# Performance work log

Measured on AMD Instinct MI355X. Metric: run time of the kernel, lower is better.

Reference implementation:

```python
import jax, jax.numpy as jnp
import numpy as np

N_NODES = 100000
IN_CH = 256
HIDDEN = 256
N_EDGES = 500000


def setup_inputs() -> dict:
    key = jax.random.key(0)
    k_emb, k_ei, k_w1, k_w2 = jax.random.split(key, 4)
    embeddings = jax.random.normal(k_emb, (N_NODES, IN_CH), dtype=jnp.float32)
    edge_index = jax.random.randint(k_ei, (2, N_EDGES), 0, N_NODES, dtype=jnp.int64)
    # Linear(in*2, hidden) and Linear(hidden, 1) weights (stored input-major for x @ W)
    s1 = 1.0 / np.sqrt(2 * IN_CH)
    s2 = 1.0 / np.sqrt(HIDDEN)
    W1 = jax.random.uniform(k_w1, (2 * IN_CH, HIDDEN), dtype=jnp.float32, minval=-s1, maxval=s1)
    b1 = jnp.zeros((HIDDEN,), dtype=jnp.float32)
    W2 = jax.random.uniform(k_w2, (HIDDEN, 1), dtype=jnp.float32, minval=-s2, maxval=s2)
    b2 = jnp.zeros((1,), dtype=jnp.float32)
    return {"embeddings": embeddings, "edge_index": edge_index,
            "W1": W1, "b1": b1, "W2": W2, "b2": b2}


def reference(embeddings, edge_index, W1, b1, W2, b2):
    src, dst = edge_index[0], edge_index[1]
    # gather [E, in] twice, concat -> [E, 2*in]
    feats = jnp.concatenate([embeddings[src], embeddings[dst]], axis=-1)
    h = jax.nn.relu(feats @ W1 + b1)          # [E, hidden]
    scores = h @ W2 + b2                      # [E, 1]
    return scores.reshape(-1)
```

## Files before the change

### kernel.cpp

```cpp
#include <hip/hip_runtime.h>
#include <hip/hip_bf16.h>

#define NN   100000
#define EE   500000
#define MPAD 100096

using bf16x8 = __attribute__((ext_vector_type(8))) short;
using f32x4  = __attribute__((ext_vector_type(4))) float;
using u16x8  = __attribute__((ext_vector_type(8))) unsigned short;

__device__ __forceinline__ unsigned short f2bf(float f) {
  unsigned int x = __builtin_bit_cast(unsigned int, f);
  x += 0x7fffu + ((x >> 16) & 1u);
  return (unsigned short)(x >> 16);
}
__device__ __forceinline__ float bf2f(unsigned short u) {
  unsigned int x = ((unsigned int)u) << 16;
  return __builtin_bit_cast(float, x);
}
__device__ __forceinline__ unsigned short f2bh(float f) {
  return __builtin_bit_cast(unsigned short, __float2bfloat16(f));
}
__device__ __forceinline__ void glds16(const void* g, const void* l) {
  __builtin_amdgcn_global_load_lds((const __attribute__((address_space(1))) void*)g,
                                   (__attribute__((address_space(3))) void*)l, 16, 0, 0);
}

__global__ void wprep_kernel(const float* __restrict__ W1, unsigned short* __restrict__ WT) {
  int id = blockIdx.x * blockDim.x + threadIdx.x;
  if (id >= 512 * 32) return;
  int j  = id >> 5;
  int cg = id & 31;
  int jc = j & 255;
  int kb = (cg << 3) + ((j >= 256) ? 256 : 0);
  u16x8 v;
#pragma unroll
  for (int t = 0; t < 8; ++t)
    v[t] = f2bf(W1[(size_t)(kb + t) * 256 + jc]);
  *reinterpret_cast<u16x8*>(WT + (size_t)j * 256 + (cg << 3)) = v;
}

__global__ __launch_bounds__(256, 4) void gemm_pq(const float* __restrict__ emb,
                                                  const unsigned short* __restrict__ WT,
                                                  const float* __restrict__ b1,
                                                  unsigned short* __restrict__ R) {
  __shared__ unsigned short ldsA[2][128 * 32];
  __shared__ unsigned short ldsB[2][128 * 32];

  const int t    = threadIdx.x;
  const int lane = t & 63;
  const int wave = t >> 6;
  const int wrow = wave >> 1, wcol = wave & 1;
  const int bid = (int)blockIdx.x;
  const int lid = (bid & 7) * 391 + (bid >> 3);
  const int m0 = (lid >> 2) * 128;
  const int n0 = (lid & 3) * 128;

  const int a_r = t >> 1, a_h = t & 1;
  int arow_g = m0 + a_r; if (arow_g >= NN) arow_g = NN - 1;
  const float* aSrc = emb + (size_t)arow_g * 256 + (a_h << 4);
  const int a_s  = (a_r >> 1) & 3;
  const int aW0  = a_r * 32 + ((((a_h << 1) | 0) ^ a_s) << 3);
  const int aW1  = a_r * 32 + ((((a_h << 1) | 1) ^ a_s) << 3);

  size_t bOff[2]; int bLds[2];
#pragma unroll
  for (int i = 0; i < 2; ++i) {
    const int r  = wave * 32 + i * 16 + (lane >> 2);
    const int qp = lane & 3;
    const int g  = qp ^ ((r >> 1) & 3);
    bOff[i] = (size_t)(n0 + r) * 256 + (g << 3);
    bLds[i] = (wave * 32 + i * 16) * 32;
  }

  const int fr = lane & 15, fq = lane >> 4;
  int aoff[4], boff[4];
#pragma unroll
  for (int m = 0; m < 4; ++m) {
    const int r = wrow * 64 + 16 * m + fr;
    aoff[m] = r * 32 + ((fq ^ ((r >> 1) & 3)) << 3);
  }
#pragma unroll
  for (int n = 0; n < 4; ++n) {
    const int r = wcol * 64 + 16 * n + fr;
    boff[n] = r * 32 + ((fq ^ ((r >> 1) & 3)) << 3);
  }

  f32x4 acc[4][4] = {};
  float4 pA[4];

#define ALOAD(kb)                                                              \
  do {                                                                         \
    pA[0] = *(const float4*)(aSrc + (kb));                                     \
    pA[1] = *(const float4*)(aSrc + (kb) + 4);                                 \
    pA[2] = *(const float4*)(aSrc + (kb) + 8);                                 \
    pA[3] = *(const float4*)(aSrc + (kb) + 12);                                \
  } while (0)

#define AWRITE(buf)                                                            \
  do {                                                                         \
    u16x8 w0, w1;                                                              \
    w0[0] = f2bh(pA[0].x); w0[1] = f2bh(pA[0].y);                              \
    w0[2] = f2bh(pA[0].z); w0[3] = f2bh(pA[0].w);                              \
    w0[4] = f2bh(pA[1].x); w0[5] = f2bh(pA[1].y);                              \
    w0[6] = f2bh(pA[1].z); w0[7] = f2bh(pA[1].w);                              \
    w1[0] = f2bh(pA[2].x); w1[1] = f2bh(pA[2].y);                              \
    w1[2] = f2bh(pA[2].z); w1[3] = f2bh(pA[2].w);                              \
    w1[4] = f2bh(pA[3].x); w1[5] = f2bh(pA[3].y);                              \
    w1[6] = f2bh(pA[3].z); w1[7] = f2bh(pA[3].w);                              \
    *(u16x8*)&ldsA[(buf)][aW0] = w0;                                           \
    *(u16x8*)&ldsA[(buf)][aW1] = w1;                                           \
  } while (0)

#define BGLDS(buf, kb)                                                         \
  do {                                                                         \
    glds16(WT + bOff[0] + (kb), &ldsB[(buf)][bLds[0]]);                        \
    glds16(WT + bOff[1] + (kb), &ldsB[(buf)][bLds[1]]);                        \
  } while (0)

  ALOAD(0);
  AWRITE(0);
  BGLDS(0, 0);
  ALOAD(32);
  __syncthreads();

#pragma unroll
  for (int ks = 0; ks < 8; ++ks) {
    const int p = ks & 1;
    if (ks < 7) {
      BGLDS(p ^ 1, (ks + 1) * 32);
      AWRITE(p ^ 1);
      if (ks < 6) ALOAD((ks + 2) * 32);
    }
    bf16x8 av[4], bv[4];
#pragma unroll
    for (int m = 0; m < 4; ++m) av[m] = *(const bf16x8*)&ldsA[p][aoff[m]];
#pragma unroll
    for (int n = 0; n < 4; ++n) bv[n] = *(const bf16x8*)&ldsB[p][boff[n]];
#pragma unroll
    for (int m = 0; m < 4; ++m)
#pragma unroll
      for (int n = 0; n < 4; ++n)
        acc[m][n] = __builtin_amdgcn_mfma_f32_16x16x32_bf16(av[m], bv[n], acc[m][n], 0, 0, 0);
    if (ks < 7) __syncthreads();
  }

  float bn[4];
#pragma unroll
  for (int n = 0; n < 4; ++n) {
    const int c = n0 + wcol * 64 + 16 * n + fr;
    bn[n] = (c < 256) ? b1[c] : 0.f;
  }
#pragma unroll
  for (int m = 0; m < 4; ++m) {
    const int r0 = m0 + wrow * 64 + 16 * m + (fq << 2);
#pragma unroll
    for (int n = 0; n < 4; ++n) {
      const int c = n0 + wcol * 64 + 16 * n + fr;
#pragma unroll
      for (int i = 0; i < 4; ++i)
        R[(size_t)(r0 + i) * 512 + c] = f2bh(acc[m][n][i] + bn[n]);
    }
  }
#undef ALOAD
#undef AWRITE
#undef BGLDS
}

__global__ __launch_bounds__(256) void edge_kernel(const int* __restrict__ idx,
                                                   const unsigned short* __restrict__ R,
                                                   const float* __restrict__ W2,
                                                   const float* __restrict__ b2,
                                                   float* __restrict__ out) {
  const int lane  = threadIdx.x & 63;
  const int half  = lane >> 5;
  const int l     = lane & 31;
  const int gwave = (int)((blockIdx.x * blockDim.x + threadIdx.x) >> 6);
  const int nwave = (int)((gridDim.x * blockDim.x) >> 6);
  const float4 w0 = *(const float4*)(W2 + (l << 3));
  const float4 w1 = *(const float4*)(W2 + (l << 3) + 4);
  const float bias = b2[0];

  for (int c = gwave; c < (EE / 8); c += nwave) {
    const int e0 = c << 3;
    int s[4], d[4];
#pragma unroll
    for (int u = 0; u < 4; ++u) {
      s[u] = idx[e0 + (u << 1) + half];
      d[u] = idx[EE + e0 + (u << 1) + half];
    }
    u16x8 ga[4], gb[4];
#pragma unroll
    for (int u = 0; u < 4; ++u) {
      ga[u] = *(const u16x8*)(R + (size_t)s[u] * 512 + (l << 3));
      gb[u] = *(const u16x8*)(R + (size_t)d[u] * 512 + 256 + (l << 3));
    }
#pragma unroll
    for (int u = 0; u < 4; ++u) {
      float acc;
      acc  = fmaxf(bf2f((unsigned short)ga[u][0]) + bf2f((unsigned short)gb[u][0]), 0.f) * w0.x;
      acc += fmaxf(bf2f((unsigned short)ga[u][1]) + bf2f((unsigned short)gb[u][1]), 0.f) * w0.y;
      acc += fmaxf(bf2f((unsigned short)ga[u][2]) + bf2f((unsigned short)gb[u][2]), 0.f) * w0.z;
      acc += fmaxf(bf2f((unsigned short)ga[u][3]) + bf2f((unsigned short)gb[u][3]), 0.f) * w0.w;
      acc += fmaxf(bf2f((unsigned short)ga[u][4]) + bf2f((unsigned short)gb[u][4]), 0.f) * w1.x;
      acc += fmaxf(bf2f((unsigned short)ga[u][5]) + bf2f((unsigned short)gb[u][5]), 0.f) * w1.y;
      acc += fmaxf(bf2f((unsigned short)ga[u][6]) + bf2f((unsigned short)gb[u][6]), 0.f) * w1.z;
      acc += fmaxf(bf2f((unsigned short)ga[u][7]) + bf2f((unsigned short)gb[u][7]), 0.f) * w1.w;
#pragma unroll
      for (int off = 16; off > 0; off >>= 1) acc += __shfl_xor(acc, off, 64);
      if (l == 0) out[e0 + (u << 1) + half] = acc + bias;
    }
  }
}

__global__ __launch_bounds__(256) void fallback_kernel(const float* __restrict__ emb,
                                                       const int* __restrict__ idx,
                                                       const float* __restrict__ W1,
                                                       const float* __restrict__ b1,
                                                       const float* __restrict__ W2,
                                                       const float* __restrict__ b2,
                                                       float* __restrict__ out) {
  __shared__ float feats[512];
  __shared__ float red[256];
  const int t = threadIdx.x;
  for (int e = blockIdx.x; e < EE; e += gridDim.x) {
    __syncthreads();
    const int s = idx[e], d = idx[EE + e];
    feats[t]       = emb[(size_t)s * 256 + t];
    feats[256 + t] = emb[(size_t)d * 256 + t];
    __syncthreads();
    float h = b1[t];
    for (int k = 0; k < 512; ++k) h += feats[k] * W1[k * 256 + t];
    red[t] = fmaxf(h, 0.f) * W2[t];
    __syncthreads();
    for (int off = 128; off > 0; off >>= 1) {
      if (t < off) red[t] += red[t + off];
      __syncthreads();
    }
    if (t == 0) out[e] = red[0] + b2[0];
  }
}

extern "C" void kernel_launch(void* const* d_in, const int* in_sizes, int n_in,
                              void* d_out, int out_size, void* d_ws, size_t ws_size,
                              hipStream_t stream) {
  const float* emb = (const float*)d_in[0];
  const int*   idx = (const int*)d_in[1];
  const float* W1  = (const float*)d_in[2];
  const float* b1  = (const float*)d_in[3];
  const float* W2  = (const float*)d_in[4];
  const float* b2  = (const float*)d_in[5];
  float* out = (float*)d_out;

  const size_t wt_elems = (size_t)512 * 256;
  const size_t r_elems  = (size_t)MPAD * 512;
  const size_t need = (wt_elems + r_elems) * sizeof(unsigned short);

  if (ws_size < need) {
    fallback_kernel<<<4096, 256, 0, stream>>>(emb, idx, W1, b1, W2, b2, out);
    return;
  }

  unsigned short* WT = (unsigned short*)d_ws;
  unsigned short* R  = WT + wt_elems;

  wprep_kernel<<<64, 256, 0, stream>>>(W1, WT);
  gemm_pq<<<(MPAD / 128) * 4, 256, 0, stream>>>(emb, WT, b1, R);
  edge_kernel<<<2048, 256, 0, stream>>>(idx, R, W2, b2, out);
}
```

Baseline: 138.8 us.

## Pre-convert embeddings to bf16 and stage GEMM A tiles via direct LDS loads

Adds a separate pass that converts the fp32 embedding table to a padded bf16 buffer in workspace. The GEMM then loads both A and B tiles with global_load_lds straight into LDS, removing the per-tile register staging and fp32-to-bf16 conversion from its main loop. Occupancy hint drops from 4 to 3 blocks. The cost is an extra kernel that reads 100MB of fp32 and writes 50MB of bf16, plus a larger workspace requirement. The old path is kept as a fallback when workspace is too small.

```diff
diff --git a/kernel.cpp b/kernel.cpp
--- a/kernel.cpp
+++ b/kernel.cpp
@@ -24,6 +24,23 @@
 __device__ __forceinline__ void glds16(const void* g, const void* l) {
   __builtin_amdgcn_global_load_lds((const __attribute__((address_space(1))) void*)g,
                                    (__attribute__((address_space(3))) void*)l, 16, 0, 0);
+}
+
+__global__ __launch_bounds__(256) void cvt_emb(const float* __restrict__ emb,
+                                               unsigned short* __restrict__ EB) {
+  const int ngrp = MPAD * 32;
+  for (int g = blockIdx.x * blockDim.x + threadIdx.x; g < ngrp;
+       g += gridDim.x * blockDim.x) {
+    const int row  = g >> 5;
+    const int col8 = (g & 31) << 3;
+    const int srow = (row < NN) ? row : (NN - 1);
+    const float4 f0 = *(const float4*)(emb + (size_t)srow * 256 + col8);
+    const float4 f1 = *(const float4*)(emb + (size_t)srow * 256 + col8 + 4);
+    u16x8 v;
+    v[0] = f2bh(f0.x); v[1] = f2bh(f0.y); v[2] = f2bh(f0.z); v[3] = f2bh(f0.w);
+    v[4] = f2bh(f1.x); v[5] = f2bh(f1.y); v[6] = f2bh(f1.z); v[7] = f2bh(f1.w);
+    *(u16x8*)(EB + (size_t)row * 256 + col8) = v;
+  }
 }
 
 __global__ void wprep_kernel(const float* __restrict__ W1, unsigned short* __restrict__ WT) {
@@ -40,7 +57,7 @@
   *reinterpret_cast<u16x8*>(WT + (size_t)j * 256 + (cg << 3)) = v;
 }
 
-__global__ __launch_bounds__(256, 4) void gemm_pq(const float* __restrict__ emb,
+__global__ __launch_bounds__(256, 3) void gemm_pq(const unsigned short* __restrict__ EB,
                                                   const unsigned short* __restrict__ WT,
                                                   const float* __restrict__ b1,
                                                   unsigned short* __restrict__ R) {
@@ -56,13 +73,100 @@
   const int m0 = (lid >> 2) * 128;
   const int n0 = (lid & 3) * 128;
 
+  size_t aOffG[2], bOffG[2]; int sLds[2];
+#pragma unroll
+  for (int i = 0; i < 2; ++i) {
+    const int r  = wave * 32 + i * 16 + (lane >> 2);
+    const int qp = lane & 3;
+    const int g  = qp ^ ((r >> 1) & 3);
+    aOffG[i] = (size_t)(m0 + r) * 256 + (g << 3);
+    bOffG[i] = (size_t)(n0 + r) * 256 + (g << 3);
+    sLds[i]  = (wave * 32 + i * 16) * 32;
+  }
+
+  const int fr = lane & 15, fq = lane >> 4;
+  int aoff[4], boff[4];
+#pragma unroll
+  for (int m = 0; m < 4; ++m) {
+    const int r = wrow * 64 + 16 * m + fr;
+    aoff[m] = r * 32 + ((fq ^ ((r >> 1) & 3)) << 3);
+  }
+#pragma unroll
+  for (int n = 0; n < 4; ++n) {
+    const int r = wcol * 64 + 16 * n + fr;
+    boff[n] = r * 32 + ((fq ^ ((r >> 1) & 3)) << 3);
+  }
+
+#define STAGE(buf, kb)                                                         \
+  do {                                                                         \
+    glds16(EB + aOffG[0] + (kb), &ldsA[(buf)][sLds[0]]);                       \
+    glds16(EB + aOffG[1] + (kb), &ldsA[(buf)][sLds[1]]);                       \
+    glds16(WT + bOffG[0] + (kb), &ldsB[(buf)][sLds[0]]);                       \
+    glds16(WT + bOffG[1] + (kb), &ldsB[(buf)][sLds[1]]);                       \
+  } while (0)
+
+  f32x4 acc[4][4] = {};
+
+  STAGE(0, 0);
+  __syncthreads();
+
+#pragma unroll
+  for (int ks = 0; ks < 8; ++ks) {
+    const int p = ks & 1;
+    if (ks < 7) STAGE(p ^ 1, (ks + 1) * 32);
+    bf16x8 av[4], bv[4];
+#pragma unroll
+    for (int m = 0; m < 4; ++m) av[m] = *(const bf16x8*)&ldsA[p][aoff[m]];
+#pragma unroll
+    for (int n = 0; n < 4; ++n) bv[n] = *(const bf16x8*)&ldsB[p][boff[n]];
+#pragma unroll
+    for (int m = 0; m < 4; ++m)
+#pragma unroll
+      for (int n = 0; n < 4; ++n)
+        acc[m][n] = __builtin_amdgcn_mfma_f32_16x16x32_bf16(av[m], bv[n], acc[m][n], 0, 0, 0);
+    if (ks < 7) __syncthreads();
+  }
+
+  float bn[4];
+#pragma unroll
+  for (int n = 0; n < 4; ++n) {
+    const int c = n0 + wcol * 64 + 16 * n + fr;
+    bn[n] = (c < 256) ? b1[c] : 0.f;
+  }
+#pragma unroll
+  for (int m = 0; m < 4; ++m) {
+    const int r0 = m0 + wrow * 64 + 16 * m + (fq << 2);
+#pragma unroll
+    for (int n = 0; n < 4; ++n) {
+      const int c = n0 + wcol * 64 + 16 * n + fr;
+#pragma unroll
+      for (int i = 0; i < 4; ++i)
+        R[(size_t)(r0 + i) * 512 + c] = f2bh(acc[m][n][i] + bn[n]);
+    }
+  }
+#undef STAGE
+}
+
+__global__ __launch_bounds__(256, 3) void gemm_pq_r5(const float* __restrict__ emb,
+                                                     const unsigned short* __restrict__ WT,
+                                                     const float* __restrict__ b1,
+                                                     unsigned short* __restrict__ R) {
+  __shared__ unsigned short ldsA[2][128 * 32];
+  __shared__ unsigned short ldsB[2][128 * 32];
+  const int t    = threadIdx.x;
+  const int lane = t & 63;
+  const int wave = t >> 6;
+  const int wrow = wave >> 1, wcol = wave & 1;
+  const int bid = (int)blockIdx.x;
+  const int lid = (bid & 7) * 391 + (bid >> 3);
+  const int m0 = (lid >> 2) * 128;
+  const int n0 = (lid & 3) * 128;
   const int a_r = t >> 1, a_h = t & 1;
   int arow_g = m0 + a_r; if (arow_g >= NN) arow_g = NN - 1;
   const float* aSrc = emb + (size_t)arow_g * 256 + (a_h << 4);
   const int a_s  = (a_r >> 1) & 3;
   const int aW0  = a_r * 32 + ((((a_h << 1) | 0) ^ a_s) << 3);
   const int aW1  = a_r * 32 + ((((a_h << 1) | 1) ^ a_s) << 3);
-
   size_t bOff[2]; int bLds[2];
 #pragma unroll
   for (int i = 0; i < 2; ++i) {
@@ -72,7 +176,6 @@
     bOff[i] = (size_t)(n0 + r) * 256 + (g << 3);
     bLds[i] = (wave * 32 + i * 16) * 32;
   }
-
   const int fr = lane & 15, fq = lane >> 4;
   int aoff[4], boff[4];
 #pragma unroll
@@ -85,21 +188,15 @@
     const int r = wcol * 64 + 16 * n + fr;
     boff[n] = r * 32 + ((fq ^ ((r >> 1) & 3)) << 3);
   }
-
   f32x4 acc[4][4] = {};
   float4 pA[4];
-
 #define ALOAD(kb)                                                              \
-  do {                                                                         \
-    pA[0] = *(const float4*)(aSrc + (kb));                                     \
-    pA[1] = *(const float4*)(aSrc + (kb) + 4);                                 \
-    pA[2] = *(const float4*)(aSrc + (kb) + 8);                                 \
-    pA[3] = *(const float4*)(aSrc + (kb) + 12);                                \
-  } while (0)
-
+  do { pA[0] = *(const float4*)(aSrc + (kb));                                  \
+       pA[1] = *(const float4*)(aSrc + (kb) + 4);                              \
+       pA[2] = *(const float4*)(aSrc + (kb) + 8);                              \
+       pA[3] = *(const float4*)(aSrc + (kb) + 12); } while (0)
 #define AWRITE(buf)                                                            \
-  do {                                                                         \
-    u16x8 w0, w1;                                                              \
+  do { u16x8 w0, w1;                                                           \
     w0[0] = f2bh(pA[0].x); w0[1] = f2bh(pA[0].y);                              \
     w0[2] = f2bh(pA[0].z); w0[3] = f2bh(pA[0].w);                              \
     w0[4] = f2bh(pA[1].x); w0[5] = f2bh(pA[1].y);                              \
@@ -109,21 +206,12 @@
     w1[4] = f2bh(pA[3].x); w1[5] = f2bh(pA[3].y);                              \
     w1[6] = f2bh(pA[3].z); w1[7] = f2bh(pA[3].w);                              \
     *(u16x8*)&ldsA[(buf)][aW0] = w0;                                           \
-    *(u16x8*)&ldsA[(buf)][aW1] = w1;                                           \
-  } while (0)
-
+    *(u16x8*)&ldsA[(buf)][aW1] = w1; } while (0)
 #define BGLDS(buf, kb)                                                         \
-  do {                                                                         \
-    glds16(WT + bOff[0] + (kb), &ldsB[(buf)][bLds[0]]);                        \
-    glds16(WT + bOff[1] + (kb), &ldsB[(buf)][bLds[1]]);                        \
-  } while (0)
-
-  ALOAD(0);
-  AWRITE(0);
-  BGLDS(0, 0);
-  ALOAD(32);
+  do { glds16(WT + bOff[0] + (kb), &ldsB[(buf)][bLds[0]]);                     \
+       glds16(WT + bOff[1] + (kb), &ldsB[(buf)][bLds[1]]); } while (0)
+  ALOAD(0); AWRITE(0); BGLDS(0, 0); ALOAD(32);
   __syncthreads();
-
 #pragma unroll
   for (int ks = 0; ks < 8; ++ks) {
     const int p = ks & 1;
@@ -144,7 +232,6 @@
         acc[m][n] = __builtin_amdgcn_mfma_f32_16x16x32_bf16(av[m], bv[n], acc[m][n], 0, 0, 0);
     if (ks < 7) __syncthreads();
   }
-
   float bn[4];
 #pragma unroll
   for (int n = 0; n < 4; ++n) {
@@ -254,17 +341,24 @@
 
   const size_t wt_elems = (size_t)512 * 256;
   const size_t r_elems  = (size_t)MPAD * 512;
-  const size_t need = (wt_elems + r_elems) * sizeof(unsigned short);
-
-  if (ws_size < need) {
-    fallback_kernel<<<4096, 256, 0, stream>>>(emb, idx, W1, b1, W2, b2, out);
-    return;
-  }
+  const size_t eb_elems = (size_t)MPAD * 256;
+  const size_t need_small = (wt_elems + r_elems) * sizeof(unsigned short);
+  const size_t need_full  = (wt_elems + r_elems + eb_elems) * sizeof(unsigned short);
 
   unsigned short* WT = (unsigned short*)d_ws;
   unsigned short* R  = WT + wt_elems;
-
-  wprep_kernel<<<64, 256, 0, stream>>>(W1, WT);
-  gemm_pq<<<(MPAD / 128) * 4, 256, 0, stream>>>(emb, WT, b1, R);
-  edge_kernel<<<2048, 256, 0, stream>>>(idx, R, W2, b2, out);
-}
+  unsigned short* EB = R + r_elems;
+
+  if (ws_size >= need_full) {
+    wprep_kernel<<<64, 256, 0, stream>>>(W1, WT);
+    cvt_emb<<<2048, 256, 0, stream>>>(emb, EB);
+    gemm_pq<<<(MPAD / 128) * 4, 256, 0, stream>>>(EB, WT, b1, R);
+    edge_kernel<<<2048, 256, 0, stream>>>(idx, R, W2, b2, out);
+  } else if (ws_size >= need_small) {
+    wprep_kernel<<<64, 256, 0, stream>>>(W1, WT);
+    gemm_pq_r5<<<(MPAD / 128) * 4, 256, 0, stream>>>(emb, WT, b1, R);
+    edge_kernel<<<2048, 256, 0, stream>>>(idx, R, W2, b2, out);
+  } else {
+    fallback_kernel<<<4096, 256, 0, stream>>>(emb, idx, W1, b1, W2, b2, out);
+  }
+}
```

After: 146.9 us. 5.9% more time.
